# Optimization experiments

Measured on AMD Instinct MI355X. Metric: run time of the kernel, lower is better.

## Reference

```python
import jax, jax.numpy as jnp
import numpy as np

N_NODES = 50000


def graph_conv(src, dst, x, W, b, n_nodes):
    """DGL GraphConv, norm='both': D_out^{-1/2} A D_in^{-1/2} x W + b.
    src/dst: [E] edge endpoints (message flows src -> dst).
    """
    ones = jnp.ones(src.shape[0], dtype=x.dtype)
    deg_out = jnp.clip(jax.ops.segment_sum(ones, src, num_segments=n_nodes), 1.0)
    deg_in = jnp.clip(jax.ops.segment_sum(ones, dst, num_segments=n_nodes), 1.0)
    h = x * jax.lax.rsqrt(deg_out)[:, None]          # src-side normalization
    msgs = h[src]                                     # [E, F] gather (irregular)
    agg = jax.ops.segment_sum(msgs, dst, num_segments=n_nodes)  # SpMM scatter-add
    agg = agg * jax.lax.rsqrt(deg_in)[:, None]        # dst-side normalization
    return agg @ W + b


def setup_inputs() -> dict:
    key = jax.random.key(0)
    ks = jax.random.split(key, 9)
    E = 600000
    in_f, hid, emb = 128, 64, 32
    features = jax.random.normal(ks[0], (N_NODES, in_f), dtype=jnp.float32)
    src = jax.random.randint(ks[1], (E,), 0, N_NODES)
    dst = jax.random.randint(ks[2], (E,), 0, N_NODES)

    def glorot(k, fan_in, fan_out):
        lim = np.sqrt(6.0 / (fan_in + fan_out)).astype(np.float32)
        return jax.random.uniform(k, (fan_in, fan_out), jnp.float32, -lim, lim)

    return {
        "features": features, "src": src, "dst": dst,
        "W1": glorot(ks[3], in_f, hid), "b1": jnp.zeros((hid,), jnp.float32),
        "W2": glorot(ks[4], hid, emb), "b2": jnp.zeros((emb,), jnp.float32),
        "W3": glorot(ks[5], emb, in_f), "b3": jnp.zeros((in_f,), jnp.float32),
    }


def reference(features, src, dst, W1, b1, W2, b2, W3, b3):
    h = jax.nn.relu(graph_conv(src, dst, features, W1, b1, N_NODES))
    z = graph_conv(src, dst, h, W2, b2, N_NODES)
    recon = graph_conv(src, dst, z, W3, b3, N_NODES)
    return (z, recon)
```

## Files before the change

### kernel.cpp

```cpp
#include <hip/hip_runtime.h>
#include <hip/hip_bf16.h>


#define HNB 4
#define HPB 64
#define HBIN 12500
typedef unsigned short u16;

__device__ __forceinline__ float bfhi(unsigned u) {
    unsigned v = u & 0xFFFF0000u;
    return __builtin_bit_cast(float, v);
}
__device__ __forceinline__ float bflo(unsigned u) {
    unsigned v = u << 16;
    return __builtin_bit_cast(float, v);
}
__device__ __forceinline__ unsigned f2bf(float f) {
    unsigned u = __builtin_bit_cast(unsigned, f);
    return (u + 0x7FFFu + ((u >> 16) & 1u)) >> 16;
}

__global__ __launch_bounds__(256) void k_hist2(
    const int* __restrict__ src, const int* __restrict__ dst,
    u16* __restrict__ slab, int E, int slice)
{
    __shared__ int h[HBIN];
    const int which = blockIdx.x / (HNB * HPB);
    const int bin   = (blockIdx.x / HPB) % HNB;
    const int p     = blockIdx.x % HPB;
    const int* __restrict__ idx = which ? dst : src;

    for (int i = threadIdx.x; i < HBIN; i += 256) h[i] = 0;
    __syncthreads();

    const int lo  = bin * HBIN;
    const int beg = p * slice;
    const int fin = min(beg + slice, E);
    for (int i = beg + threadIdx.x * 4; i + 3 < fin; i += 1024) {
        const int4 v = *(const int4*)(idx + i);
        int u;
        u = v.x - lo; if ((unsigned)u < (unsigned)HBIN) atomicAdd(&h[u], 1);
        u = v.y - lo; if ((unsigned)u < (unsigned)HBIN) atomicAdd(&h[u], 1);
        u = v.z - lo; if ((unsigned)u < (unsigned)HBIN) atomicAdd(&h[u], 1);
        u = v.w - lo; if ((unsigned)u < (unsigned)HBIN) atomicAdd(&h[u], 1);
    }
    for (int i = beg + ((fin - beg) & ~3) + threadIdx.x; i < fin; i += 256) {
        int u = idx[i] - lo;
        if ((unsigned)u < (unsigned)HBIN) atomicAdd(&h[u], 1);
    }
    __syncthreads();

    unsigned* out = (unsigned*)(slab + (size_t)blockIdx.x * HBIN);
    for (int i = threadIdx.x; i < HBIN / 2; i += 256)
        out[i] = (unsigned)h[2 * i] | ((unsigned)h[2 * i + 1] << 16);
}

__global__ __launch_bounds__(256) void k_reduce_scan(
    u16* __restrict__ slab, float* __restrict__ rs_out, float* __restrict__ rs_in,
    int* __restrict__ partial, int* __restrict__ blocksum, int N)
{
    __shared__ int tmp[256];
    const int tid = threadIdx.x;
    const int i = blockIdx.x * 256 + tid;

    int run = 0;
    if (i < N) {
        const int bin = i / HBIN;
        const int off = i - bin * HBIN;
        const u16* s_src = slab + ((size_t)(bin * HPB)) * HBIN + off;
        u16*       s_dst = slab + ((size_t)((HNB + bin) * HPB)) * HBIN + off;

        int so = 0;
#pragma unroll
        for (int p = 0; p < HPB; ++p) so += s_src[(size_t)p * HBIN];
#pragma unroll
        for (int p = 0; p < HPB; ++p) {
            const int c = s_dst[(size_t)p * HBIN];
            s_dst[(size_t)p * HBIN] = (u16)run;
            run += c;
        }
        rs_out[i] = rsqrtf(fmaxf((float)so, 1.0f));
        rs_in[i]  = rsqrtf(fmaxf((float)run, 1.0f));
    }
    tmp[tid] = run; __syncthreads();
    for (int off = 1; off < 256; off <<= 1) {
        int t = (tid >= off) ? tmp[tid - off] : 0;
        __syncthreads(); tmp[tid] += t; __syncthreads();
    }
    if (i < N) partial[i] = tmp[tid];
    if (tid == 255) blocksum[blockIdx.x] = tmp[255];
}

__global__ void k_scan2(int* __restrict__ blocksum, int nb) {
    __shared__ int tmp[256];
    const int tid = threadIdx.x;
    int v = (tid < nb) ? blocksum[tid] : 0;
    tmp[tid] = v; __syncthreads();
    for (int off = 1; off < 256; off <<= 1) {
        int t = (tid >= off) ? tmp[tid - off] : 0;
        __syncthreads(); tmp[tid] += t; __syncthreads();
    }
    if (tid < nb) blocksum[tid] = tmp[tid];
}

__global__ void k_scan3(const int* __restrict__ partial, const int* __restrict__ blocksum,
                        int* __restrict__ row_ptr, int n) {
    const int i = blockIdx.x * 256 + threadIdx.x;
    if (i < n) {
        const int base = (blockIdx.x > 0) ? blocksum[blockIdx.x - 1] : 0;
        row_ptr[i + 1] = partial[i] + base;
        if (i == 0) row_ptr[0] = 0;
    }
}

__global__ __launch_bounds__(256) void k_fill2(
    const int* __restrict__ src, const int* __restrict__ dst,
    const int* __restrict__ row_ptr, const u16* __restrict__ slab,
    int* __restrict__ csr_src, int E, int slice, int N)
{
    __shared__ int cur[HBIN];
    const int bin = blockIdx.x / HPB;
    const int p   = blockIdx.x % HPB;
    const int lo  = bin * HBIN;

    const u16* part_off = slab + ((size_t)((HNB + bin) * HPB + p)) * HBIN;
    for (int j = threadIdx.x; j < HBIN; j += 256) {
        const int node = lo + j;
        cur[j] = (node < N) ? (row_ptr[node] + (int)part_off[j]) : 0;
    }
    __syncthreads();

    const int beg = p * slice;
    const int fin = min(beg + slice, E);
    for (int i = beg + threadIdx.x * 4; i + 3 < fin; i += 1024) {
        const int4 d = *(const int4*)(dst + i);
        const int4 s = *(const int4*)(src + i);
        int u;
        u = d.x - lo; if ((unsigned)u < (unsigned)HBIN) csr_src[atomicAdd(&cur[u], 1)] = s.x;
        u = d.y - lo; if ((unsigned)u < (unsigned)HBIN) csr_src[atomicAdd(&cur[u], 1)] = s.y;
        u = d.z - lo; if ((unsigned)u < (unsigned)HBIN) csr_src[atomicAdd(&cur[u], 1)] = s.z;
        u = d.w - lo; if ((unsigned)u < (unsigned)HBIN) csr_src[atomicAdd(&cur[u], 1)] = s.w;
    }
    for (int i = beg + ((fin - beg) & ~3) + threadIdx.x; i < fin; i += 256) {
        int u = dst[i] - lo;
        if ((unsigned)u < (unsigned)HBIN) csr_src[atomicAdd(&cur[u], 1)] = src[i];
    }
}

template <int IN_F, int OUT_F, int TM>
__global__ __launch_bounds__(256) void k_gemm_bf16out(
    const float* __restrict__ X, const float* __restrict__ W,
    const float* __restrict__ rowscale, u16* __restrict__ Y, int n)
{
    constexpr int CT  = OUT_F / 4;
    constexpr int RT  = 256 / CT;
    constexpr int RPT = TM / RT;
    constexpr int XS  = IN_F + 4;
    __shared__ float sW[IN_F * OUT_F];
    __shared__ float sX[TM * XS];
    const int tid = threadIdx.x;
    const int row0 = blockIdx.x * TM;

    for (int i = tid; i < IN_F * OUT_F / 4; i += 256)
        ((float4*)sW)[i] = ((const float4*)W)[i];
    for (int i = tid; i < TM * IN_F / 4; i += 256) {
        const int r  = i / (IN_F / 4);
        const int c4 = (i % (IN_F / 4)) * 4;
        const int gr = row0 + r;
        float4 v = make_float4(0.f, 0.f, 0.f, 0.f);
        if (gr < n) v = *(const float4*)(X + (long)gr * IN_F + c4);
        *(float4*)(sX + r * XS + c4) = v;
    }
    __syncthreads();

    const int tc = tid % CT;
    const int tr = tid / CT;
    float4 acc[RPT];
#pragma unroll
    for (int i = 0; i < RPT; ++i) acc[i] = make_float4(0.f, 0.f, 0.f, 0.f);

#pragma unroll 8
    for (int k = 0; k < IN_F; ++k) {
        const float4 w = *(const float4*)(sW + k * OUT_F + 4 * tc);
#pragma unroll
        for (int i = 0; i < RPT; ++i) {
            const float xv = sX[(tr + i * RT) * XS + k];
            acc[i].x += xv * w.x; acc[i].y += xv * w.y;
            acc[i].z += xv * w.z; acc[i].w += xv * w.w;
        }
    }

#pragma unroll
    for (int i = 0; i < RPT; ++i) {
        const int gr = row0 + tr + i * RT;
        if (gr < n) {
            float4 v = acc[i];
            const float s = rowscale[gr];
            v.x *= s; v.y *= s; v.z *= s; v.w *= s;
            uint2 pk;
            pk.x = f2bf(v.x) | (f2bf(v.y) << 16);
            pk.y = f2bf(v.z) | (f2bf(v.w) << 16);
            *(uint2*)(Y + (size_t)gr * OUT_F + 4 * tc) = pk;
        }
    }
}

__global__ __launch_bounds__(256) void k_gather_gemm_B(
    const int* __restrict__ row_ptr, const int* __restrict__ csr_src,
    const u16* __restrict__ t1b, const float* __restrict__ rs_in,
    const float* __restrict__ rs_out, const float* __restrict__ b1,
    const float* __restrict__ W2, u16* __restrict__ t2b, int N)
{
    __shared__ float sh[32][72];
    __shared__ float sW[64 * 32];
    const int tid = threadIdx.x;

    for (int i = tid; i < 64 * 32 / 4; i += 256)
        ((float4*)sW)[i] = ((const float4*)W2)[i];

    const int nloc = tid / 8;
    const int node = blockIdx.x * 32 + nloc;
    const int c8 = (tid % 8) * 8;

    float a[8];
#pragma unroll
    for (int t = 0; t < 8; ++t) a[t] = 0.f;

    if (node < N) {
        const int beg = row_ptr[node];
        const int end = row_ptr[node + 1];
        int j = beg;
        for (; j + 3 < end; j += 4) {
            const int s0 = csr_src[j], s1 = csr_src[j + 1];
            const int s2 = csr_src[j + 2], s3 = csr_src[j + 3];
            const uint4 q0 = *(const uint4*)(t1b + (size_t)s0 * 64 + c8);
            const uint4 q1 = *(const uint4*)(t1b + (size_t)s1 * 64 + c8);
            const uint4 q2 = *(const uint4*)(t1b + (size_t)s2 * 64 + c8);
            const uint4 q3 = *(const uint4*)(t1b + (size_t)s3 * 64 + c8);
            a[0] += bflo(q0.x); a[1] += bfhi(q0.x); a[2] += bflo(q0.y); a[3] += bfhi(q0.y);
            a[4] += bflo(q0.z); a[5] += bfhi(q0.z); a[6] += bflo(q0.w); a[7] += bfhi(q0.w);
            a[0] += bflo(q1.x); a[1] += bfhi(q1.x); a[2] += bflo(q1.y); a[3] += bfhi(q1.y);
            a[4] += bflo(q1.z); a[5] += bfhi(q1.z); a[6] += bflo(q1.w); a[7] += bfhi(q1.w);
            a[0] += bflo(q2.x); a[1] += bfhi(q2.x); a[2] += bflo(q2.y); a[3] += bfhi(q2.y);
            a[4] += bflo(q2.z); a[5] += bfhi(q2.z); a[6] += bflo(q2.w); a[7] += bfhi(q2.w);
            a[0] += bflo(q3.x); a[1] += bfhi(q3.x); a[2] += bflo(q3.y); a[3] += bfhi(q3.y);
            a[4] += bflo(q3.z); a[5] += bfhi(q3.z); a[6] += bflo(q3.w); a[7] += bfhi(q3.w);
        }
        for (; j < end; ++j) {
            const int s = csr_src[j];
            const uint4 q = *(const uint4*)(t1b + (size_t)s * 64 + c8);
            a[0] += bflo(q.x); a[1] += bfhi(q.x); a[2] += bflo(q.y); a[3] += bfhi(q.y);
            a[4] += bflo(q.z); a[5] += bfhi(q.z); a[6] += bflo(q.w); a[7] += bfhi(q.w);
        }
        const float rs = rs_in[node];
#pragma unroll
        for (int t = 0; t < 8; ++t)
            a[t] = fmaxf(a[t] * rs + b1[c8 + t], 0.f);
    }
#pragma unroll
    for (int t = 0; t < 8; ++t) sh[nloc][c8 + t] = a[t];
    __syncthreads();

    const int n2 = tid / 8;
    const int c4 = (tid % 8) * 4;
    float4 acc = make_float4(0.f, 0.f, 0.f, 0.f);
#pragma unroll 8
    for (int k = 0; k < 64; ++k) {
        const float xv = sh[n2][k];
        const float4 w = *(const float4*)(sW + k * 32 + c4);
        acc.x += xv * w.x; acc.y += xv * w.y; acc.z += xv * w.z; acc.w += xv * w.w;
    }
    const int gn = blockIdx.x * 32 + n2;
    if (gn < N) {
        const float s = rs_out[gn];
        uint2 pk;
        pk.x = f2bf(acc.x * s) | (f2bf(acc.y * s) << 16);
        pk.y = f2bf(acc.z * s) | (f2bf(acc.w * s) << 16);
        *(uint2*)(t2b + (size_t)gn * 32 + c4) = pk;
    }
}

__global__ __launch_bounds__(256) void k_gather_C(
    const int* __restrict__ row_ptr, const int* __restrict__ csr_src,
    const u16* __restrict__ t2b, const float* __restrict__ rs_in,
    const float* __restrict__ rs_out, const float* __restrict__ b2,
    float* __restrict__ z, u16* __restrict__ zb, int N)
{
    const int node = blockIdx.x * 64 + threadIdx.x / 4;
    const int c8 = (threadIdx.x % 4) * 8;
    if (node >= N) return;

    const int beg = row_ptr[node];
    const int end = row_ptr[node + 1];
    float a[8];
#pragma unroll
    for (int t = 0; t < 8; ++t) a[t] = 0.f;

    int j = beg;
    for (; j + 3 < end; j += 4) {
        const int s0 = csr_src[j], s1 = csr_src[j + 1];
        const int s2 = csr_src[j + 2], s3 = csr_src[j + 3];
        const uint4 q0 = *(const uint4*)(t2b + (size_t)s0 * 32 + c8);
        const uint4 q1 = *(const uint4*)(t2b + (size_t)s1 * 32 + c8);
        const uint4 q2 = *(const uint4*)(t2b + (size_t)s2 * 32 + c8);
        const uint4 q3 = *(const uint4*)(t2b + (size_t)s3 * 32 + c8);
        a[0] += bflo(q0.x); a[1] += bfhi(q0.x); a[2] += bflo(q0.y); a[3] += bfhi(q0.y);
        a[4] += bflo(q0.z); a[5] += bfhi(q0.z); a[6] += bflo(q0.w); a[7] += bfhi(q0.w);
        a[0] += bflo(q1.x); a[1] += bfhi(q1.x); a[2] += bflo(q1.y); a[3] += bfhi(q1.y);
        a[4] += bflo(q1.z); a[5] += bfhi(q1.z); a[6] += bflo(q1.w); a[7] += bfhi(q1.w);
        a[0] += bflo(q2.x); a[1] += bfhi(q2.x); a[2] += bflo(q2.y); a[3] += bfhi(q2.y);
        a[4] += bflo(q2.z); a[5] += bfhi(q2.z); a[6] += bflo(q2.w); a[7] += bfhi(q2.w);
        a[0] += bflo(q3.x); a[1] += bfhi(q3.x); a[2] += bflo(q3.y); a[3] += bfhi(q3.y);
        a[4] += bflo(q3.z); a[5] += bfhi(q3.z); a[6] += bflo(q3.w); a[7] += bfhi(q3.w);
    }
    for (; j < end; ++j) {
        const int s = csr_src[j];
        const uint4 q = *(const uint4*)(t2b + (size_t)s * 32 + c8);
        a[0] += bflo(q.x); a[1] += bfhi(q.x); a[2] += bflo(q.y); a[3] += bfhi(q.y);
        a[4] += bflo(q.z); a[5] += bfhi(q.z); a[6] += bflo(q.w); a[7] += bfhi(q.w);
    }

    const float rs = rs_in[node];
    float v[8];
#pragma unroll
    for (int t = 0; t < 8; ++t) v[t] = a[t] * rs + b2[c8 + t];

    float* o = z + (size_t)node * 32 + c8;
    *(float4*)(o)     = make_float4(v[0], v[1], v[2], v[3]);
    *(float4*)(o + 4) = make_float4(v[4], v[5], v[6], v[7]);

    const float ss = rs_out[node];
    uint4 pk;
    pk.x = f2bf(v[0] * ss) | (f2bf(v[1] * ss) << 16);
    pk.y = f2bf(v[2] * ss) | (f2bf(v[3] * ss) << 16);
    pk.z = f2bf(v[4] * ss) | (f2bf(v[5] * ss) << 16);
    pk.w = f2bf(v[6] * ss) | (f2bf(v[7] * ss) << 16);
    *(uint4*)(zb + (size_t)node * 32 + c8) = pk;
}

__global__ __launch_bounds__(256) void k_gather_gemm_D(
    const int* __restrict__ row_ptr, const int* __restrict__ csr_src,
    const u16* __restrict__ zb, const float* __restrict__ rs_in,
    const float* __restrict__ W3, const float* __restrict__ b3,
    float* __restrict__ recon, int N)
{
    __shared__ float sa[64][36];
    __shared__ float sW[32 * 128];
    const int tid = threadIdx.x;

    for (int i = tid; i < 32 * 128 / 4; i += 256)
        ((float4*)sW)[i] = ((const float4*)W3)[i];

    const int nloc = tid / 4;
    const int node = blockIdx.x * 64 + nloc;
    const int c8 = (tid % 4) * 8;

    float a[8];
#pragma unroll
    for (int t = 0; t < 8; ++t) a[t] = 0.f;

    if (node < N) {
        const int beg = row_ptr[node];
        const int end = row_ptr[node + 1];
        int j = beg;
        for (; j + 3 < end; j += 4) {
            const int s0 = csr_src[j], s1 = csr_src[j + 1];
            const int s2 = csr_src[j + 2], s3 = csr_src[j + 3];
            const uint4 q0 = *(const uint4*)(zb + (size_t)s0 * 32 + c8);
            const uint4 q1 = *(const uint4*)(zb + (size_t)s1 * 32 + c8);
            const uint4 q2 = *(const uint4*)(zb + (size_t)s2 * 32 + c8);
            const uint4 q3 = *(const uint4*)(zb + (size_t)s3 * 32 + c8);
            a[0] += bflo(q0.x); a[1] += bfhi(q0.x); a[2] += bflo(q0.y); a[3] += bfhi(q0.y);
            a[4] += bflo(q0.z); a[5] += bfhi(q0.z); a[6] += bflo(q0.w); a[7] += bfhi(q0.w);
            a[0] += bflo(q1.x); a[1] += bfhi(q1.x); a[2] += bflo(q1.y); a[3] += bfhi(q1.y);
            a[4] += bflo(q1.z); a[5] += bfhi(q1.z); a[6] += bflo(q1.w); a[7] += bfhi(q1.w);
            a[0] += bflo(q2.x); a[1] += bfhi(q2.x); a[2] += bflo(q2.y); a[3] += bfhi(q2.y);
            a[4] += bflo(q2.z); a[5] += bfhi(q2.z); a[6] += bflo(q2.w); a[7] += bfhi(q2.w);
            a[0] += bflo(q3.x); a[1] += bfhi(q3.x); a[2] += bflo(q3.y); a[3] += bfhi(q3.y);
            a[4] += bflo(q3.z); a[5] += bfhi(q3.z); a[6] += bflo(q3.w); a[7] += bfhi(q3.w);
        }
        for (; j < end; ++j) {
            const int s = csr_src[j];
            const uint4 q = *(const uint4*)(zb + (size_t)s * 32 + c8);
            a[0] += bflo(q.x); a[1] += bfhi(q.x); a[2] += bflo(q.y); a[3] += bfhi(q.y);
            a[4] += bflo(q.z); a[5] += bfhi(q.z); a[6] += bflo(q.w); a[7] += bfhi(q.w);
        }
        const float rs = rs_in[node];
#pragma unroll
        for (int t = 0; t < 8; ++t) a[t] *= rs;
    }
#pragma unroll
    for (int t = 0; t < 8; ++t) sa[nloc][c8 + t] = a[t];
    __syncthreads();

    const int ng = (tid / 32) * 8;
    const int c4 = (tid % 32) * 4;
    const float4 bb = *(const float4*)(b3 + c4);
    float4 acc[8];
#pragma unroll
    for (int i = 0; i < 8; ++i) acc[i] = bb;
#pragma unroll 4
    for (int k = 0; k < 32; ++k) {
        const float4 w = *(const float4*)(sW + k * 128 + c4);
#pragma unroll
        for (int i = 0; i < 8; ++i) {
            const float xv = sa[ng + i][k];
            acc[i].x += xv * w.x; acc[i].y += xv * w.y;
            acc[i].z += xv * w.z; acc[i].w += xv * w.w;
        }
    }
#pragma unroll
    for (int i = 0; i < 8; ++i) {
        const int gn = blockIdx.x * 64 + ng + i;
        if (gn < N) *(float4*)(recon + (size_t)gn * 128 + c4) = acc[i];
    }
}

extern "C" void kernel_launch(void* const* d_in, const int* in_sizes, int n_in,
                              void* d_out, int out_size, void* d_ws, size_t ws_size,
                              hipStream_t stream) {
    const float* feat = (const float*)d_in[0];
    const int*   src  = (const int*)d_in[1];
    const int*   dst  = (const int*)d_in[2];
    const float* W1   = (const float*)d_in[3];
    const float* b1   = (const float*)d_in[4];
    const float* W2   = (const float*)d_in[5];
    const float* b2   = (const float*)d_in[6];
    const float* W3   = (const float*)d_in[7];
    const float* b3   = (const float*)d_in[8];

    const int E = in_sizes[1];
    const int N = in_sizes[0] / 128;
    const int slice = (((E + HPB - 1) / HPB) + 3) & ~3;

    const size_t SLABN = 2UL * HNB * HPB * HBIN;
    u16* slab     = (u16*)d_ws;
    int* row_ptr  = (int*)(slab + SLABN);
    int* scan_p   = row_ptr + N + 16;
    int* blocksum = scan_p + N;
    int* csr_src  = blocksum + 256;
    float* rs_out = (float*)(csr_src + E);
    float* rs_in  = rs_out + N;
    u16* t2b      = (u16*)(rs_in + N);
    u16* zb       = t2b + (size_t)N * 32;
    u16* t1b      = (u16*)slab;

    float* z_out  = (float*)d_out;
    float* recon  = z_out + (size_t)N * 32;

    const int B = 256;
    const int nb_scan = (N + 255) / 256;

    k_hist2<<<2 * HNB * HPB, B, 0, stream>>>(src, dst, slab, E, slice);
    k_reduce_scan<<<nb_scan, B, 0, stream>>>(slab, rs_out, rs_in, scan_p, blocksum, N);
    k_scan2<<<1, B, 0, stream>>>(blocksum, nb_scan);
    k_scan3<<<nb_scan, B, 0, stream>>>(scan_p, blocksum, row_ptr, N);
    k_fill2<<<HNB * HPB, B, 0, stream>>>(src, dst, row_ptr, slab, csr_src, E, slice, N);

    k_gemm_bf16out<128, 64, 32><<<(N + 31) / 32, B, 0, stream>>>(
        feat, W1, rs_out, t1b, N);

    k_gather_gemm_B<<<(N + 31) / 32, B, 0, stream>>>(
        row_ptr, csr_src, t1b, rs_in, rs_out, b1, W2, t2b, N);

    k_gather_C<<<(N + 63) / 64, B, 0, stream>>>(
        row_ptr, csr_src, t2b, rs_in, rs_out, b2, z_out, zb, N);

    k_gather_gemm_D<<<(N + 63) / 64, B, 0, stream>>>(
        row_ptr, csr_src, zb, rs_in, W3, b3, recon, N);
}
```

Before: 212.7 us.

## Use packed full-range histogram, merge scan kernels, split edge lists across two lanes

```diff
diff --git a/kernel.cpp b/kernel.cpp
--- a/kernel.cpp
+++ b/kernel.cpp
@@ -2,9 +2,10 @@
 #include <hip/hip_bf16.h>
 
 
-#define HNB 4
-#define HPB 64
-#define HBIN 12500
+#define NN   50000
+#define HPB  128
+#define FNB  4
+#define FBIN 12500
 typedef unsigned short u16;
 
 __device__ __forceinline__ float bfhi(unsigned u) {
@@ -20,39 +21,35 @@
     return (u + 0x7FFFu + ((u >> 16) & 1u)) >> 16;
 }
 
-__global__ __launch_bounds__(256) void k_hist2(
+__global__ __launch_bounds__(256) void k_hist1(
     const int* __restrict__ src, const int* __restrict__ dst,
     u16* __restrict__ slab, int E, int slice)
 {
-    __shared__ int h[HBIN];
-    const int which = blockIdx.x / (HNB * HPB);
-    const int bin   = (blockIdx.x / HPB) % HNB;
+    __shared__ unsigned h[NN / 2];
+    const int which = blockIdx.x / HPB;
     const int p     = blockIdx.x % HPB;
     const int* __restrict__ idx = which ? dst : src;
 
-    for (int i = threadIdx.x; i < HBIN; i += 256) h[i] = 0;
-    __syncthreads();
-
-    const int lo  = bin * HBIN;
+    for (int i = threadIdx.x; i < NN / 2; i += 256) h[i] = 0;
+    __syncthreads();
+
     const int beg = p * slice;
     const int fin = min(beg + slice, E);
     for (int i = beg + threadIdx.x * 4; i + 3 < fin; i += 1024) {
         const int4 v = *(const int4*)(idx + i);
-        int u;
-        u = v.x - lo; if ((unsigned)u < (unsigned)HBIN) atomicAdd(&h[u], 1);
-        u = v.y - lo; if ((unsigned)u < (unsigned)HBIN) atomicAdd(&h[u], 1);
-        u = v.z - lo; if ((unsigned)u < (unsigned)HBIN) atomicAdd(&h[u], 1);
-        u = v.w - lo; if ((unsigned)u < (unsigned)HBIN) atomicAdd(&h[u], 1);
+        atomicAdd(&h[v.x >> 1], 1u << ((v.x & 1) << 4));
+        atomicAdd(&h[v.y >> 1], 1u << ((v.y & 1) << 4));
+        atomicAdd(&h[v.z >> 1], 1u << ((v.z & 1) << 4));
+        atomicAdd(&h[v.w >> 1], 1u << ((v.w & 1) << 4));
     }
     for (int i = beg + ((fin - beg) & ~3) + threadIdx.x; i < fin; i += 256) {
-        int u = idx[i] - lo;
-        if ((unsigned)u < (unsigned)HBIN) atomicAdd(&h[u], 1);
-    }
-    __syncthreads();
-
-    unsigned* out = (unsigned*)(slab + (size_t)blockIdx.x * HBIN);
-    for (int i = threadIdx.x; i < HBIN / 2; i += 256)
-        out[i] = (unsigned)h[2 * i] | ((unsigned)h[2 * i + 1] << 16);
+        const int u = idx[i];
+        atomicAdd(&h[u >> 1], 1u << ((u & 1) << 4));
+    }
+    __syncthreads();
+
+    unsigned* out = (unsigned*)(slab + (size_t)blockIdx.x * NN);
+    for (int i = threadIdx.x; i < NN / 2; i += 256) out[i] = h[i];
 }
 
 __global__ __launch_bounds__(256) void k_reduce_scan(
@@ -65,18 +62,15 @@
 
     int run = 0;
     if (i < N) {
-        const int bin = i / HBIN;
-        const int off = i - bin * HBIN;
-        const u16* s_src = slab + ((size_t)(bin * HPB)) * HBIN + off;
-        u16*       s_dst = slab + ((size_t)((HNB + bin) * HPB)) * HBIN + off;
-
+        const u16* s_src = slab + i;
+        u16*       s_dst = slab + (size_t)HPB * NN + i;
         int so = 0;
-#pragma unroll
-        for (int p = 0; p < HPB; ++p) so += s_src[(size_t)p * HBIN];
-#pragma unroll
+#pragma unroll 8
+        for (int p = 0; p < HPB; ++p) so += s_src[(size_t)p * NN];
+#pragma unroll 8
         for (int p = 0; p < HPB; ++p) {
-            const int c = s_dst[(size_t)p * HBIN];
-            s_dst[(size_t)p * HBIN] = (u16)run;
+            const int c = s_dst[(size_t)p * NN];
+            s_dst[(size_t)p * NN] = (u16)run;
             run += c;
         }
         rs_out[i] = rsqrtf(fmaxf((float)so, 1.0f));
@@ -91,7 +85,10 @@
     if (tid == 255) blocksum[blockIdx.x] = tmp[255];
 }
 
-__global__ void k_scan2(int* __restrict__ blocksum, int nb) {
+__global__ __launch_bounds__(256) void k_scan23(
+    const int* __restrict__ partial, const int* __restrict__ blocksum,
+    int* __restrict__ row_ptr, int n, int nb)
+{
     __shared__ int tmp[256];
     const int tid = threadIdx.x;
     int v = (tid < nb) ? blocksum[tid] : 0;
@@ -100,14 +97,10 @@
         int t = (tid >= off) ? tmp[tid - off] : 0;
         __syncthreads(); tmp[tid] += t; __syncthreads();
     }
-    if (tid < nb) blocksum[tid] = tmp[tid];
-}
-
-__global__ void k_scan3(const int* __restrict__ partial, const int* __restrict__ blocksum,
-                        int* __restrict__ row_ptr, int n) {
-    const int i = blockIdx.x * 256 + threadIdx.x;
+    __syncthreads();
+    const int i = blockIdx.x * 256 + tid;
     if (i < n) {
-        const int base = (blockIdx.x > 0) ? blocksum[blockIdx.x - 1] : 0;
+        const int base = (blockIdx.x > 0) ? tmp[blockIdx.x - 1] : 0;
         row_ptr[i + 1] = partial[i] + base;
         if (i == 0) row_ptr[0] = 0;
     }
@@ -118,15 +111,15 @@
     const int* __restrict__ row_ptr, const u16* __restrict__ slab,
     int* __restrict__ csr_src, int E, int slice, int N)
 {
-    __shared__ int cur[HBIN];
+    __shared__ int cur[FBIN];
     const int bin = blockIdx.x / HPB;
     const int p   = blockIdx.x % HPB;
-    const int lo  = bin * HBIN;
-
-    const u16* part_off = slab + ((size_t)((HNB + bin) * HPB + p)) * HBIN;
-    for (int j = threadIdx.x; j < HBIN; j += 256) {
+    const int lo  = bin * FBIN;
+
+    const u16* part_off = slab + (size_t)(HPB + p) * NN;
+    for (int j = threadIdx.x; j < FBIN; j += 256) {
         const int node = lo + j;
-        cur[j] = (node < N) ? (row_ptr[node] + (int)part_off[j]) : 0;
+        cur[j] = (node < N) ? (row_ptr[node] + (int)part_off[node]) : 0;
     }
     __syncthreads();
 
@@ -136,14 +129,14 @@
         const int4 d = *(const int4*)(dst + i);
         const int4 s = *(const int4*)(src + i);
         int u;
-        u = d.x - lo; if ((unsigned)u < (unsigned)HBIN) csr_src[atomicAdd(&cur[u], 1)] = s.x;
-        u = d.y - lo; if ((unsigned)u < (unsigned)HBIN) csr_src[atomicAdd(&cur[u], 1)] = s.y;
-        u = d.z - lo; if ((unsigned)u < (unsigned)HBIN) csr_src[atomicAdd(&cur[u], 1)] = s.z;
-        u = d.w - lo; if ((unsigned)u < (unsigned)HBIN) csr_src[atomicAdd(&cur[u], 1)] = s.w;
+        u = d.x - lo; if ((unsigned)u < (unsigned)FBIN) csr_src[atomicAdd(&cur[u], 1)] = s.x;
+        u = d.y - lo; if ((unsigned)u < (unsigned)FBIN) csr_src[atomicAdd(&cur[u], 1)] = s.y;
+        u = d.z - lo; if ((unsigned)u < (unsigned)FBIN) csr_src[atomicAdd(&cur[u], 1)] = s.z;
+        u = d.w - lo; if ((unsigned)u < (unsigned)FBIN) csr_src[atomicAdd(&cur[u], 1)] = s.w;
     }
     for (int i = beg + ((fin - beg) & ~3) + threadIdx.x; i < fin; i += 256) {
         int u = dst[i] - lo;
-        if ((unsigned)u < (unsigned)HBIN) csr_src[atomicAdd(&cur[u], 1)] = src[i];
+        if ((unsigned)u < (unsigned)FBIN) csr_src[atomicAdd(&cur[u], 1)] = src[i];
     }
 }
 
@@ -205,22 +198,28 @@
     }
 }
 
+#define ACC8(q) do { \
+    a[0] += bflo((q).x); a[1] += bfhi((q).x); a[2] += bflo((q).y); a[3] += bfhi((q).y); \
+    a[4] += bflo((q).z); a[5] += bfhi((q).z); a[6] += bflo((q).w); a[7] += bfhi((q).w); } while (0)
+
 __global__ __launch_bounds__(256) void k_gather_gemm_B(
     const int* __restrict__ row_ptr, const int* __restrict__ csr_src,
     const u16* __restrict__ t1b, const float* __restrict__ rs_in,
     const float* __restrict__ rs_out, const float* __restrict__ b1,
     const float* __restrict__ W2, u16* __restrict__ t2b, int N)
 {
-    __shared__ float sh[32][72];
+    __shared__ float sh[16][72];
     __shared__ float sW[64 * 32];
     const int tid = threadIdx.x;
 
     for (int i = tid; i < 64 * 32 / 4; i += 256)
         ((float4*)sW)[i] = ((const float4*)W2)[i];
 
-    const int nloc = tid / 8;
-    const int node = blockIdx.x * 32 + nloc;
-    const int c8 = (tid % 8) * 8;
+    const int nloc = tid >> 4;
+    const int sub  = tid & 15;
+    const int half = sub >> 3;
+    const int c8   = (sub & 7) * 8;
+    const int node = blockIdx.x * 16 + nloc;
 
     float a[8];
 #pragma unroll
@@ -229,54 +228,52 @@
     if (node < N) {
         const int beg = row_ptr[node];
         const int end = row_ptr[node + 1];
-        int j = beg;
-        for (; j + 3 < end; j += 4) {
+        const int len0 = (end - beg + 1) >> 1;
+        int j        = half ? beg + len0 : beg;
+        const int je = half ? end : beg + len0;
+        for (; j + 3 < je; j += 4) {
             const int s0 = csr_src[j], s1 = csr_src[j + 1];
             const int s2 = csr_src[j + 2], s3 = csr_src[j + 3];
             const uint4 q0 = *(const uint4*)(t1b + (size_t)s0 * 64 + c8);
             const uint4 q1 = *(const uint4*)(t1b + (size_t)s1 * 64 + c8);
             const uint4 q2 = *(const uint4*)(t1b + (size_t)s2 * 64 + c8);
             const uint4 q3 = *(const uint4*)(t1b + (size_t)s3 * 64 + c8);
-            a[0] += bflo(q0.x); a[1] += bfhi(q0.x); a[2] += bflo(q0.y); a[3] += bfhi(q0.y);
-            a[4] += bflo(q0.z); a[5] += bfhi(q0.z); a[6] += bflo(q0.w); a[7] += bfhi(q0.w);
-            a[0] += bflo(q1.x); a[1] += bfhi(q1.x); a[2] += bflo(q1.y); a[3] += bfhi(q1.y);
-            a[4] += bflo(q1.z); a[5] += bfhi(q1.z); a[6] += bflo(q1.w); a[7] += bfhi(q1.w);
-            a[0] += bflo(q2.x); a[1] += bfhi(q2.x); a[2] += bflo(q2.y); a[3] += bfhi(q2.y);
-            a[4] += bflo(q2.z); a[5] += bfhi(q2.z); a[6] += bflo(q2.w); a[7] += bfhi(q2.w);
-            a[0] += bflo(q3.x); a[1] += bfhi(q3.x); a[2] += bflo(q3.y); a[3] += bfhi(q3.y);
-            a[4] += bflo(q3.z); a[5] += bfhi(q3.z); a[6] += bflo(q3.w); a[7] += bfhi(q3.w);
-        }
-        for (; j < end; ++j) {
-            const int s = csr_src[j];
-            const uint4 q = *(const uint4*)(t1b + (size_t)s * 64 + c8);
-            a[0] += bflo(q.x); a[1] += bfhi(q.x); a[2] += bflo(q.y); a[3] += bfhi(q.y);
-            a[4] += bflo(q.z); a[5] += bfhi(q.z); a[6] += bflo(q.w); a[7] += bfhi(q.w);
-        }
+            ACC8(q0); ACC8(q1); ACC8(q2); ACC8(q3);
+        }
+        for (; j < je; ++j) {
+            const uint4 q = *(const uint4*)(t1b + (size_t)csr_src[j] * 64 + c8);
+            ACC8(q);
+        }
+    }
+#pragma unroll
+    for (int t = 0; t < 8; ++t) a[t] += __shfl_xor(a[t], 8);
+
+    if (node < N && half == 0) {
         const float rs = rs_in[node];
 #pragma unroll
         for (int t = 0; t < 8; ++t)
-            a[t] = fmaxf(a[t] * rs + b1[c8 + t], 0.f);
-    }
-#pragma unroll
-    for (int t = 0; t < 8; ++t) sh[nloc][c8 + t] = a[t];
-    __syncthreads();
-
-    const int n2 = tid / 8;
-    const int c4 = (tid % 8) * 4;
-    float4 acc = make_float4(0.f, 0.f, 0.f, 0.f);
+            sh[nloc][c8 + t] = fmaxf(a[t] * rs + b1[c8 + t], 0.f);
+    }
+    __syncthreads();
+
+    if (tid < 128) {
+        const int n2 = tid >> 3;
+        const int c4 = (tid & 7) * 4;
+        float4 acc = make_float4(0.f, 0.f, 0.f, 0.f);
 #pragma unroll 8
-    for (int k = 0; k < 64; ++k) {
-        const float xv = sh[n2][k];
-        const float4 w = *(const float4*)(sW + k * 32 + c4);
-        acc.x += xv * w.x; acc.y += xv * w.y; acc.z += xv * w.z; acc.w += xv * w.w;
-    }
-    const int gn = blockIdx.x * 32 + n2;
-    if (gn < N) {
-        const float s = rs_out[gn];
-        uint2 pk;
-        pk.x = f2bf(acc.x * s) | (f2bf(acc.y * s) << 16);
-        pk.y = f2bf(acc.z * s) | (f2bf(acc.w * s) << 16);
-        *(uint2*)(t2b + (size_t)gn * 32 + c4) = pk;
+        for (int k = 0; k < 64; ++k) {
+            const float xv = sh[n2][k];
+            const float4 w = *(const float4*)(sW + k * 32 + c4);
+            acc.x += xv * w.x; acc.y += xv * w.y; acc.z += xv * w.z; acc.w += xv * w.w;
+        }
+        const int gn = blockIdx.x * 16 + n2;
+        if (gn < N) {
+            const float s = rs_out[gn];
+            uint2 pk;
+            pk.x = f2bf(acc.x * s) | (f2bf(acc.y * s) << 16);
+            pk.y = f2bf(acc.z * s) | (f2bf(acc.w * s) << 16);
+            *(uint2*)(t2b + (size_t)gn * 32 + c4) = pk;
+        }
     }
 }
 
@@ -286,39 +283,38 @@
     const float* __restrict__ rs_out, const float* __restrict__ b2,
     float* __restrict__ z, u16* __restrict__ zb, int N)
 {
-    const int node = blockIdx.x * 64 + threadIdx.x / 4;
-    const int c8 = (threadIdx.x % 4) * 8;
+    const int node = blockIdx.x * 32 + (threadIdx.x >> 3);
+    const int sub  = threadIdx.x & 7;
+    const int half = sub >> 2;
+    const int c8   = (sub & 3) * 8;
     if (node >= N) return;
 
     const int beg = row_ptr[node];
     const int end = row_ptr[node + 1];
+    const int len0 = (end - beg + 1) >> 1;
+    int j        = half ? beg + len0 : beg;
+    const int je = half ? end : beg + len0;
+
     float a[8];
 #pragma unroll
     for (int t = 0; t < 8; ++t) a[t] = 0.f;
 
-    int j = beg;
-    for (; j + 3 < end; j += 4) {
+    for (; j + 3 < je; j += 4) {
         const int s0 = csr_src[j], s1 = csr_src[j + 1];
         const int s2 = csr_src[j + 2], s3 = csr_src[j + 3];
         const uint4 q0 = *(const uint4*)(t2b + (size_t)s0 * 32 + c8);
         const uint4 q1 = *(const uint4*)(t2b + (size_t)s1 * 32 + c8);
         const uint4 q2 = *(const uint4*)(t2b + (size_t)s2 * 32 + c8);
         const uint4 q3 = *(const uint4*)(t2b + (size_t)s3 * 32 + c8);
-        a[0] += bflo(q0.x); a[1] += bfhi(q0.x); a[2] += bflo(q0.y); a[3] += bfhi(q0.y);
-        a[4] += bflo(q0.z); a[5] += bfhi(q0.z); a[6] += bflo(q0.w); a[7] += bfhi(q0.w);
-        a[0] += bflo(q1.x); a[1] += bfhi(q1.x); a[2] += bflo(q1.y); a[3] += bfhi(q1.y);
-        a[4] += bflo(q1.z); a[5] += bfhi(q1.z); a[6] += bflo(q1.w); a[7] += bfhi(q1.w);
-        a[0] += bflo(q2.x); a[1] += bfhi(q2.x); a[2] += bflo(q2.y); a[3] += bfhi(q2.y);
-        a[4] += bflo(q2.z); a[5] += bfhi(q2.z); a[6] += bflo(q2.w); a[7] += bfhi(q2.w);
-        a[0] += bflo(q3.x); a[1] += bfhi(q3.x); a[2] += bflo(q3.y); a[3] += bfhi(q3.y);
-        a[4] += bflo(q3.z); a[5] += bfhi(q3.z); a[6] += bflo(q3.w); a[7] += bfhi(q3.w);
-    }
-    for (; j < end; ++j) {
-        const int s = csr_src[j];
-        const uint4 q = *(const uint4*)(t2b + (size_t)s * 32 + c8);
-        a[0] += bflo(q.x); a[1] += bfhi(q.x); a[2] += bflo(q.y); a[3] += bfhi(q.y);
-        a[4] += bflo(q.z); a[5] += bfhi(q.z); a[6] += bflo(q.w); a[7] += bfhi(q.w);
-    }
+        ACC8(q0); ACC8(q1); ACC8(q2); ACC8(q3);
+    }
+    for (; j < je; ++j) {
+        const uint4 q = *(const uint4*)(t2b + (size_t)csr_src[j] * 32 + c8);
+        ACC8(q);
+    }
+#pragma unroll
+    for (int t = 0; t < 8; ++t) a[t] += __shfl_xor(a[t], 4);
+    if (half) return;
 
     const float rs = rs_in[node];
     float v[8];
@@ -344,16 +340,18 @@
     const float* __restrict__ W3, const float* __restrict__ b3,
     float* __restrict__ recon, int N)
 {
-    __shared__ float sa[64][36];
+    __shared__ float sa[32][36];
     __shared__ float sW[32 * 128];
     const int tid = threadIdx.x;
 
     for (int i = tid; i < 32 * 128 / 4; i += 256)
         ((float4*)sW)[i] = ((const float4*)W3)[i];
 
-    const int nloc = tid / 4;
-    const int node = blockIdx.x * 64 + nloc;
-    const int c8 = (tid % 4) * 8;
+    const int nloc = tid >> 3;
+    const int sub  = tid & 7;
+    const int half = sub >> 2;
+    const int c8   = (sub & 3) * 8;
+    const int node = blockIdx.x * 32 + nloc;
 
     float a[8];
 #pragma unroll
@@ -362,56 +360,52 @@
     if (node < N) {
         const int beg = row_ptr[node];
         const int end = row_ptr[node + 1];
-        int j = beg;
-        for (; j + 3 < end; j += 4) {
+        const int len0 = (end - beg + 1) >> 1;
+        int j        = half ? beg + len0 : beg;
+        const int je = half ? end : beg + len0;
+        for (; j + 3 < je; j += 4) {
             const int s0 = csr_src[j], s1 = csr_src[j + 1];
             const int s2 = csr_src[j + 2], s3 = csr_src[j + 3];
             const uint4 q0 = *(const uint4*)(zb + (size_t)s0 * 32 + c8);
             const uint4 q1 = *(const uint4*)(zb + (size_t)s1 * 32 + c8);
             const uint4 q2 = *(const uint4*)(zb + (size_t)s2 * 32 + c8);
             const uint4 q3 = *(const uint4*)(zb + (size_t)s3 * 32 + c8);
-            a[0] += bflo(q0.x); a[1] += bfhi(q0.x); a[2] += bflo(q0.y); a[3] += bfhi(q0.y);
-            a[4] += bflo(q0.z); a[5] += bfhi(q0.z); a[6] += bflo(q0.w); a[7] += bfhi(q0.w);
-            a[0] += bflo(q1.x); a[1] += bfhi(q1.x); a[2] += bflo(q1.y); a[3] += bfhi(q1.y);
-            a[4] += bflo(q1.z); a[5] += bfhi(q1.z); a[6] += bflo(q1.w); a[7] += bfhi(q1.w);
-            a[0] += bflo(q2.x); a[1] += bfhi(q2.x); a[2] += bflo(q2.y); a[3] += bfhi(q2.y);
-            a[4] += bflo(q2.z); a[5] += bfhi(q2.z); a[6] += bflo(q2.w); a[7] += bfhi(q2.w);
-            a[0] += bflo(q3.x); a[1] += bfhi(q3.x); a[2] += bflo(q3.y); a[3] += bfhi(q3.y);
-            a[4] += bflo(q3.z); a[5] += bfhi(q3.z); a[6] += bflo(q3.w); a[7] += bfhi(q3.w);
-        }
-        for (; j < end; ++j) {
-            const int s = csr_src[j];
-            const uint4 q = *(const uint4*)(zb + (size_t)s * 32 + c8);
-            a[0] += bflo(q.x); a[1] += bfhi(q.x); a[2] += bflo(q.y); a[3] += bfhi(q.y);
-            a[4] += bflo(q.z); a[5] += bfhi(q.z); a[6] += bflo(q.w); a[7] += bfhi(q.w);
-        }
+            ACC8(q0); ACC8(q1); ACC8(q2); ACC8(q3);
+        }
+        for (; j < je; ++j) {
+            const uint4 q = *(const uint4*)(zb + (size_t)csr_src[j] * 32 + c8);
+            ACC8(q);
+        }
+    }
+#pragma unroll
+    for (int t = 0; t < 8; ++t) a[t] += __shfl_xor(a[t], 4);
+
+    if (node < N && half == 0) {
         const float rs = rs_in[node];
 #pragma unroll
-        for (int t = 0; t < 8; ++t) a[t] *= rs;
-    }
-#pragma unroll
-    for (int t = 0; t < 8; ++t) sa[nloc][c8 + t] = a[t];
-    __syncthreads();
-
-    const int ng = (tid / 32) * 8;
-    const int c4 = (tid % 32) * 4;
+        for (int t = 0; t < 8; ++t) sa[nloc][c8 + t] = a[t] * rs;
+    }
+    __syncthreads();
+
+    const int ng = (tid >> 5) * 4;
+    const int c4 = (tid & 31) * 4;
     const float4 bb = *(const float4*)(b3 + c4);
-    float4 acc[8];
-#pragma unroll
-    for (int i = 0; i < 8; ++i) acc[i] = bb;
+    float4 acc[4];
+#pragma unroll
+    for (int i = 0; i < 4; ++i) acc[i] = bb;
 #pragma unroll 4
     for (int k = 0; k < 32; ++k) {
         const float4 w = *(const float4*)(sW + k * 128 + c4);
 #pragma unroll
-        for (int i = 0; i < 8; ++i) {
+        for (int i = 0; i < 4; ++i) {
             const float xv = sa[ng + i][k];
             acc[i].x += xv * w.x; acc[i].y += xv * w.y;
             acc[i].z += xv * w.z; acc[i].w += xv * w.w;
         }
     }
 #pragma unroll
-    for (int i = 0; i < 8; ++i) {
-        const int gn = blockIdx.x * 64 + ng + i;
+    for (int i = 0; i < 4; ++i) {
+        const int gn = blockIdx.x * 32 + ng + i;
         if (gn < N) *(float4*)(recon + (size_t)gn * 128 + c4) = acc[i];
     }
 }
@@ -433,7 +427,7 @@
     const int N = in_sizes[0] / 128;
     const int slice = (((E + HPB - 1) / HPB) + 3) & ~3;
 
-    const size_t SLABN = 2UL * HNB * HPB * HBIN;
+    const size_t SLABN = 2UL * HPB * NN;
     u16* slab     = (u16*)d_ws;
     int* row_ptr  = (int*)(slab + SLABN);
     int* scan_p   = row_ptr + N + 16;
@@ -451,21 +445,20 @@
     const int B = 256;
     const int nb_scan = (N + 255) / 256;
 
-    k_hist2<<<2 * HNB * HPB, B, 0, stream>>>(src, dst, slab, E, slice);
+    k_hist1<<<2 * HPB, B, 0, stream>>>(src, dst, slab, E, slice);
     k_reduce_scan<<<nb_scan, B, 0, stream>>>(slab, rs_out, rs_in, scan_p, blocksum, N);
-    k_scan2<<<1, B, 0, stream>>>(blocksum, nb_scan);
-    k_scan3<<<nb_scan, B, 0, stream>>>(scan_p, blocksum, row_ptr, N);
-    k_fill2<<<HNB * HPB, B, 0, stream>>>(src, dst, row_ptr, slab, csr_src, E, slice, N);
+    k_scan23<<<nb_scan, B, 0, stream>>>(scan_p, blocksum, row_ptr, N, nb_scan);
+    k_fill2<<<FNB * HPB, B, 0, stream>>>(src, dst, row_ptr, slab, csr_src, E, slice, N);
 
     k_gemm_bf16out<128, 64, 32><<<(N + 31) / 32, B, 0, stream>>>(
         feat, W1, rs_out, t1b, N);
 
-    k_gather_gemm_B<<<(N + 31) / 32, B, 0, stream>>>(
+    k_gather_gemm_B<<<(N + 15) / 16, B, 0, stream>>>(
         row_ptr, csr_src, t1b, rs_in, rs_out, b1, W2, t2b, N);
 
-    k_gather_C<<<(N + 63) / 64, B, 0, stream>>>(
+    k_gather_C<<<(N + 31) / 32, B, 0, stream>>>(
         row_ptr, csr_src, t2b, rs_in, rs_out, b2, z_out, zb, N);
 
-    k_gather_gemm_D<<<(N + 63) / 64, B, 0, stream>>>(
+    k_gather_gemm_D<<<(N + 31) / 32, B, 0, stream>>>(
         row_ptr, csr_src, zb, rs_in, W3, b3, recon, N);
 }
```

Result: faster. 202.5 us (-4.8%).
